# Kernel tuning notes

Measured on AMD Instinct MI355X. Metric: run time of the kernel, lower is better.

Reference implementation:

```python
import jax, jax.numpy as jnp
import numpy as np

N = 8192
F_IN = 256
F_OUT = 128
NEG_BIG = -9.0e15


def setup_inputs() -> dict:
    key = jax.random.key(0)
    k1, k2, k3, k4 = jax.random.split(key, 4)
    x = jax.random.normal(k1, (N, F_IN), dtype=jnp.float32)
    W = jax.random.normal(k2, (F_IN, F_OUT), dtype=jnp.float32) * 0.05
    a = jax.random.normal(k3, (2 * F_OUT, 1), dtype=jnp.float32) * 0.05
    adj = jax.random.randint(k4, (N, N), 0, 2, dtype=jnp.int32)
    return {"x": x, "W": W, "a": a, "adj": adj}


def reference(x, W, a, adj):
    # h = x @ W : [N, F_OUT]
    h = x @ W
    # Original builds [N, N, 2F] concat then matmuls with a. Since
    # a_input[i,j] = concat(h_i, h_j), the score is separable:
    # (a_input @ a)[i,j] = h_i . a[:F] + h_j . a[F:]
    a1 = a[:F_OUT, 0]   # [F_OUT]
    a2 = a[F_OUT:, 0]   # [F_OUT]
    s1 = h @ a1         # [N]
    s2 = h @ a2         # [N]
    e = jax.nn.leaky_relu(s1[:, None] + s2[None, :], negative_slope=0.2)
    e = jnp.where(adj > 0, e, jnp.float32(NEG_BIG))
    attention = jax.nn.softmax(e, axis=1)   # [N, N]
    h_prime = attention @ h                 # [N, F_OUT]
    return jax.nn.elu(h_prime)
```

## Files before the change

### kernel.cpp

```cpp
#include <hip/hip_runtime.h>
#include <math.h>

#define NN 8192

typedef __attribute__((ext_vector_type(8))) short short8;
typedef __attribute__((ext_vector_type(4))) short short4v;
typedef __attribute__((ext_vector_type(4))) float f32x4;
typedef __attribute__((ext_vector_type(4))) int int4v;

#define L2E 1.4426950408889634f

typedef __attribute__((address_space(3))) unsigned lds_u32;
typedef __attribute__((address_space(1))) unsigned g_u32;

__device__ __forceinline__ void gll16(const void* g, void* l) {
    __builtin_amdgcn_global_load_lds((const g_u32*)g, (lds_u32*)l, 16, 0, 0);
}

__device__ __forceinline__ short f2bf(float f) {
    union { float f; unsigned u; } v; v.f = f;
    unsigned r = v.u + 0x7fffu + ((v.u >> 16) & 1u);
    return (short)(r >> 16);
}

__device__ __forceinline__ f32x4 zero4() {
    f32x4 v; v[0] = 0.f; v[1] = 0.f; v[2] = 0.f; v[3] = 0.f; return v;
}

__global__ void k0_wt(const float* __restrict__ W, short* __restrict__ WT) {
    int idx = blockIdx.x * 256 + threadIdx.x;
    if (idx < 256 * 128) {
        int k = idx & 255;
        int f = idx >> 8;
        WT[f * 256 + k] = f2bf(W[k * 128 + f]);
    }
}

__global__ __launch_bounds__(128) void k1_h(
        const float* __restrict__ x, const short* __restrict__ WT,
        const float* __restrict__ a, short* __restrict__ hT,
        float* __restrict__ s1L2E, float* __restrict__ s2L2E) {
    const int w = threadIdx.x >> 6;
    const int l = threadIdx.x & 63;
    const int quad = l >> 4;
    const int fr = l & 15;
    const int i0 = blockIdx.x * 32 + w * 16;

    f32x4 acc[8];
#pragma unroll
    for (int t = 0; t < 8; ++t) acc[t] = zero4();

    const float* xrow = x + (size_t)(i0 + fr) * 256;
#pragma unroll
    for (int kk = 0; kk < 8; ++kk) {
        const int k0 = kk * 32 + quad * 8;
        f32x4 xa = *(const f32x4*)(xrow + k0);
        f32x4 xb = *(const f32x4*)(xrow + k0 + 4);
        short8 av;
#pragma unroll
        for (int e = 0; e < 4; ++e) { av[e] = f2bf(xa[e]); av[4 + e] = f2bf(xb[e]); }
#pragma unroll
        for (int t = 0; t < 8; ++t) {
            short8 bv = *(const short8*)(WT + (t * 16 + fr) * 256 + k0);
            acc[t] = __builtin_amdgcn_mfma_f32_16x16x32_bf16(av, bv, acc[t], 0, 0, 0);
        }
    }

    float s1p[4] = {0.f, 0.f, 0.f, 0.f};
    float s2p[4] = {0.f, 0.f, 0.f, 0.f};
#pragma unroll
    for (int t = 0; t < 8; ++t) {
        float a1v = a[t * 16 + fr];
        float a2v = a[128 + t * 16 + fr];
#pragma unroll
        for (int r = 0; r < 4; ++r) {
            s1p[r] += acc[t][r] * a1v;
            s2p[r] += acc[t][r] * a2v;
        }
    }
#pragma unroll
    for (int r = 0; r < 4; ++r) {
#pragma unroll
        for (int m = 1; m < 16; m <<= 1) {
            s1p[r] += __shfl_xor(s1p[r], m, 64);
            s2p[r] += __shfl_xor(s2p[r], m, 64);
        }
    }
    if (fr == 0) {
#pragma unroll
        for (int r = 0; r < 4; ++r) {
            const int i = i0 + quad * 4 + r;
            s1L2E[i] = s1p[r] * L2E;
            s2L2E[i] = s2p[r] * L2E;
        }
    }

#pragma unroll
    for (int t = 0; t < 8; ++t) {
        short4v hv;
#pragma unroll
        for (int r = 0; r < 4; ++r) hv[r] = f2bf(acc[t][r]);
        *(short4v*)(hT + (size_t)(t * 16 + fr) * NN + i0 + quad * 4) = hv;
    }
}

template<int JSPLIT, bool PARTIAL>
__global__ __launch_bounds__(256, 2) void k2_attn(
        const int* __restrict__ adj, const short* __restrict__ hT,
        const float* __restrict__ s1g, const float* __restrict__ s2g,
        float* __restrict__ pvp, float* __restrict__ zp,
        float* __restrict__ out) {
    constexpr int JW = NN / JSPLIT;
    constexpr int NSTEP = JW / 64;
    constexpr int BUFB = 33792;
    __shared__ __align__(16) char lds_c[2 * BUFB + 512];

    const int tid = threadIdx.x;
    const int w = tid >> 6;
    const int l = tid & 63;
    const int quad = l >> 4;
    const int fr = l & 15;
    const int rh = w >> 1;
    const int wj = w & 1;
    const int rb = blockIdx.x / JSPLIT;
    const int jb = blockIdx.x % JSPLIT;
    const int r64 = rb * 64;
    const int jbb = jb * JW;

    const float S0 = s1g[r64 + rh * 32 + fr];
    const float S1 = s1g[r64 + rh * 32 + 16 + fr];

    const char* hsrc[4];
    const char* asrc[4];
    {
        const char* hbase = (const char*)hT;
        const char* abase = (const char*)adj;
#pragma unroll
        for (int p = 0; p < 4; ++p) {
            const int off = w * 4096 + p * 1024 + l * 16;
            {
                const int row = off >> 7;
                const int colb = off & 127;
                hsrc[p] = hbase + (size_t)row * (NN * 2) + (size_t)jbb * 2
                        + (colb ^ ((row & 7) << 4));
            }
            {
                const int row = off >> 8;
                const int colb = off & 255;
                asrc[p] = abase + (size_t)(r64 + row) * (NN * 4) + (size_t)jbb * 4
                        + (colb ^ ((row & 7) << 4));
            }
        }
    }
    const char* csrc = (const char*)s2g + (size_t)jbb * 4 + l * 16;

    auto STAGE = [&](int jt, int buf) {
        jt = (jt < NSTEP) ? jt : NSTEP - 1;
        char* hd = lds_c + buf * BUFB + w * 4096;
        char* ad = lds_c + buf * BUFB + 16384 + w * 4096;
        char* cd = lds_c + buf * BUFB + 32768;
        const size_t hof = (size_t)jt * 128;
        const size_t aof = (size_t)jt * 256;
#pragma unroll
        for (int p = 0; p < 4; ++p) gll16(hsrc[p] + hof, hd + p * 1024);
#pragma unroll
        for (int p = 0; p < 4; ++p) gll16(asrc[p] + aof, ad + p * 1024);
        gll16(csrc + aof, cd);
    };

    f32x4 acc[2][8];
#pragma unroll
    for (int m = 0; m < 2; ++m)
#pragma unroll
        for (int t = 0; t < 8; ++t) acc[m][t] = zero4();
    float zacc0 = 0.f, zacc1 = 0.f;

    STAGE(0, 0); STAGE(1, 1);

    const int ar0 = rh * 32 + fr;
    const int ar1 = rh * 32 + 16 + fr;
    const unsigned aswz = (unsigned)((ar0 & 7) << 4);
    const unsigned a0 = (unsigned)(ar0 * 256 + wj * 128 + quad * 32);
    const unsigned a1 = (unsigned)(ar1 * 256 + wj * 128 + quad * 32);

    for (int t = 0; t < NSTEP; ++t) {
        const int cur = t & 1;
        asm volatile("s_waitcnt vmcnt(9)" ::: "memory");
        __builtin_amdgcn_s_barrier();
        __builtin_amdgcn_sched_barrier(0);

        const char* hb = lds_c + cur * BUFB;
        const char* ab = lds_c + cur * BUFB + 16384;
        const float* cb = (const float*)(lds_c + cur * BUFB + 32768);

        const int4v g00 = *(const int4v*)(ab + (a0 ^ aswz));
        const int4v g01 = *(const int4v*)(ab + ((a0 + 16) ^ aswz));
        const int4v g10 = *(const int4v*)(ab + (a1 ^ aswz));
        const int4v g11 = *(const int4v*)(ab + ((a1 + 16) ^ aswz));
        const f32x4 c0 = *(const f32x4*)((const char*)cb + wj * 128 + quad * 32);
        const f32x4 c1 = *(const f32x4*)((const char*)cb + wj * 128 + quad * 32 + 16);

        short8 pa0, pa1;
        {
            float zs0 = 0.f, zs1 = 0.f;
#pragma unroll
            for (int e = 0; e < 8; ++e) {
                const float cv = (e < 4) ? c0[e] : c1[e - 4];
                const int gv0 = (e < 4) ? g00[e] : g01[e - 4];
                const int gv1 = (e < 4) ? g10[e] : g11[e - 4];
                const float u0 = S0 + cv;
                const float u1 = S1 + cv;
                const float t0 = fmaxf(u0, 0.2f * u0);
                const float t1 = fmaxf(u1, 0.2f * u1);
                const float p0 = (gv0 > 0) ? exp2f(t0) : 0.f;
                const float p1 = (gv1 > 0) ? exp2f(t1) : 0.f;
                zs0 += p0; zs1 += p1;
                pa0[e] = f2bf(p0);
                pa1[e] = f2bf(p1);
            }
            zacc0 += zs0; zacc1 += zs1;
        }

#pragma unroll
        for (int t8 = 0; t8 < 8; ++t8) {
            const int hrow = t8 * 16 + fr;
            const short8 bv = *(const short8*)(
                hb + ((unsigned)(hrow * 128 + wj * 64 + quad * 16) ^ ((hrow & 7) << 4)));
            acc[0][t8] = __builtin_amdgcn_mfma_f32_16x16x32_bf16(pa0, bv, acc[0][t8], 0, 0, 0);
            acc[1][t8] = __builtin_amdgcn_mfma_f32_16x16x32_bf16(pa1, bv, acc[1][t8], 0, 0, 0);
        }

        __builtin_amdgcn_sched_barrier(0);
        __builtin_amdgcn_s_barrier();
        STAGE(t + 2, cur);
    }

    asm volatile("s_waitcnt vmcnt(0)" ::: "memory");
    __syncthreads();

    zacc0 += __shfl_xor(zacc0, 16, 64);
    zacc0 += __shfl_xor(zacc0, 32, 64);
    zacc1 += __shfl_xor(zacc1, 16, 64);
    zacc1 += __shfl_xor(zacc1, 32, 64);
    float* zb = (float*)(lds_c + 2 * BUFB);
    if (l < 16) {
        zb[w * 32 + l] = zacc0;
        zb[w * 32 + 16 + l] = zacc1;
    }

    float* red = (float*)lds_c;
    if (wj == 1) {
#pragma unroll
        for (int m = 0; m < 2; ++m)
#pragma unroll
            for (int t8 = 0; t8 < 8; ++t8)
                *(f32x4*)(red + rh * 4096 + (m * 8 + t8) * 256 + l * 4) = acc[m][t8];
    }
    __syncthreads();

    if (wj == 0) {
#pragma unroll
        for (int m = 0; m < 2; ++m)
#pragma unroll
            for (int t8 = 0; t8 < 8; ++t8)
                acc[m][t8] += *(const f32x4*)(red + rh * 4096 + (m * 8 + t8) * 256 + l * 4);
#pragma unroll
        for (int m = 0; m < 2; ++m) {
#pragma unroll
            for (int r = 0; r < 4; ++r) {
                const int rr = m * 16 + quad * 4 + r;
                const float z = zb[(rh * 2 + 0) * 32 + rr] + zb[(rh * 2 + 1) * 32 + rr];
                const int grow = r64 + rh * 32 + rr;
                if (PARTIAL) {
                    if (fr == 0) zp[(size_t)jb * NN + grow] = z;
                    float* orow = pvp + ((size_t)jb * NN + grow) * 128;
#pragma unroll
                    for (int t8 = 0; t8 < 8; ++t8) orow[t8 * 16 + fr] = acc[m][t8][r];
                } else {
                    const float inv = 1.0f / z;
                    float* orow = out + (size_t)grow * 128;
#pragma unroll
                    for (int t8 = 0; t8 < 8; ++t8) {
                        float v = acc[m][t8][r] * inv;
                        orow[t8 * 16 + fr] = (v > 0.f) ? v : expm1f(v);
                    }
                }
            }
        }
    }
}

__global__ __launch_bounds__(256) void k3_fin(
        const float* __restrict__ pvp, const float* __restrict__ zp,
        float* __restrict__ out, int jsplit) {
    const int idx = blockIdx.x * 256 + threadIdx.x;
    const int row = idx >> 5;
    const int c = (idx & 31) << 2;
    f32x4 s = zero4();
    float z = 0.f;
    for (int p = 0; p < jsplit; ++p) {
        s += *(const f32x4*)(pvp + ((size_t)p * NN + row) * 128 + c);
        z += zp[(size_t)p * NN + row];
    }
    const float inv = 1.0f / z;
    f32x4 o;
#pragma unroll
    for (int e = 0; e < 4; ++e) {
        float v = s[e] * inv;
        o[e] = (v > 0.f) ? v : expm1f(v);
    }
    *(f32x4*)(out + (size_t)row * 128 + c) = o;
}

extern "C" void kernel_launch(void* const* d_in, const int* in_sizes, int n_in,
                              void* d_out, int out_size, void* d_ws, size_t ws_size,
                              hipStream_t stream) {
    const float* x   = (const float*)d_in[0];
    const float* W   = (const float*)d_in[1];
    const float* a   = (const float*)d_in[2];
    const int*   adj = (const int*)d_in[3];
    float* out = (float*)d_out;

    char* ws = (char*)d_ws;
    const size_t MB = 1024 * 1024;
    short* hT    = (short*)ws;
    float* s1L2E = (float*)(ws + 2 * MB);
    float* s2L2E = (float*)(ws + 2 * MB + 32768);
    short* WT    = (short*)(ws + 2 * MB + 65536);
    const size_t base = 2 * MB + 131072;

    auto need = [&](size_t js) {
        return base + js * ((size_t)NN * 128 * 4) + js * ((size_t)NN * 4);
    };
    int jsplit;
    if (ws_size >= need(4)) jsplit = 4;
    else if (ws_size >= need(2)) jsplit = 2;
    else if (ws_size >= need(1)) jsplit = 1;
    else jsplit = 0;

    float* pvp = (float*)(ws + base);
    float* zp  = (float*)(ws + base + (size_t)(jsplit > 0 ? jsplit : 1) * NN * 128 * 4);

    k0_wt<<<128, 256, 0, stream>>>(W, WT);
    k1_h<<<256, 128, 0, stream>>>(x, WT, a, hT, s1L2E, s2L2E);

    if (jsplit == 4) {
        k2_attn<4, true><<<512, 256, 0, stream>>>(adj, hT, s1L2E, s2L2E, pvp, zp, nullptr);
        k3_fin<<<1024, 256, 0, stream>>>(pvp, zp, out, 4);
    } else if (jsplit == 2) {
        k2_attn<2, true><<<256, 256, 0, stream>>>(adj, hT, s1L2E, s2L2E, pvp, zp, nullptr);
        k3_fin<<<1024, 256, 0, stream>>>(pvp, zp, out, 2);
    } else if (jsplit == 1) {
        k2_attn<1, true><<<128, 256, 0, stream>>>(adj, hT, s1L2E, s2L2E, pvp, zp, nullptr);
        k3_fin<<<1024, 256, 0, stream>>>(pvp, zp, out, 1);
    } else {
        k2_attn<1, false><<<128, 256, 0, stream>>>(adj, hT, s1L2E, s2L2E, nullptr, nullptr, out);
    }
}
```

Baseline: 83.91 us.

## Pack adjacency into a bitmask in a separate pass before attention

Adds a pre-pass kernel that converts the int32 adjacency matrix into 32-bit bitmasks. The attention kernel then reads mask bits directly from global memory instead of staging int32 adjacency tiles through LDS. LDS use drops to a double-buffered h tile and occupancy is raised to three blocks per CU. The full adjacency read still happens in the pack kernel, and the change adds a launch plus more workspace, which could shift the split choice.

```diff
diff --git a/kernel.cpp b/kernel.cpp
--- a/kernel.cpp
+++ b/kernel.cpp
@@ -33,6 +33,26 @@
         int k = idx & 255;
         int f = idx >> 8;
         WT[f * 256 + k] = f2bf(W[k * 128 + f]);
+    }
+}
+
+__global__ __launch_bounds__(256) void k_pack(
+        const int* __restrict__ adj, unsigned* __restrict__ bm32) {
+    const size_t tid = (size_t)blockIdx.x * 256 + threadIdx.x;
+    const size_t nthr = (size_t)gridDim.x * 256;
+    const size_t NW = (size_t)NN * NN / 32;
+    for (size_t wdx = tid; wdx < NW; wdx += nthr) {
+        const int4v* p = (const int4v*)(adj + wdx * 32);
+        int4v v[8];
+#pragma unroll
+        for (int q = 0; q < 8; ++q) v[q] = p[q];
+        unsigned b = 0;
+#pragma unroll
+        for (int q = 0; q < 8; ++q)
+#pragma unroll
+            for (int e = 0; e < 4; ++e)
+                b |= (v[q][e] > 0 ? 1u : 0u) << (q * 4 + e);
+        bm32[wdx] = b;
     }
 }
 
@@ -105,15 +125,14 @@
 }
 
 template<int JSPLIT, bool PARTIAL>
-__global__ __launch_bounds__(256, 2) void k2_attn(
-        const int* __restrict__ adj, const short* __restrict__ hT,
+__global__ __launch_bounds__(256, 3) void k2_attn(
+        const unsigned* __restrict__ bm32, const short* __restrict__ hT,
         const float* __restrict__ s1g, const float* __restrict__ s2g,
         float* __restrict__ pvp, float* __restrict__ zp,
         float* __restrict__ out) {
     constexpr int JW = NN / JSPLIT;
     constexpr int NSTEP = JW / 64;
-    constexpr int BUFB = 33792;
-    __shared__ __align__(16) char lds_c[2 * BUFB + 512];
+    __shared__ __align__(16) char lds_c[32768 + 512];
 
     const int tid = threadIdx.x;
     const int w = tid >> 6;
@@ -127,46 +146,33 @@
     const int r64 = rb * 64;
     const int jbb = jb * JW;
 
-    const float S0 = s1g[r64 + rh * 32 + fr];
-    const float S1 = s1g[r64 + rh * 32 + 16 + fr];
+    const int ar0 = rh * 32 + fr;
+    const int ar1 = rh * 32 + 16 + fr;
+    const float S0 = s1g[r64 + ar0];
+    const float S1 = s1g[r64 + ar1];
 
     const char* hsrc[4];
-    const char* asrc[4];
     {
         const char* hbase = (const char*)hT;
-        const char* abase = (const char*)adj;
 #pragma unroll
         for (int p = 0; p < 4; ++p) {
             const int off = w * 4096 + p * 1024 + l * 16;
-            {
-                const int row = off >> 7;
-                const int colb = off & 127;
-                hsrc[p] = hbase + (size_t)row * (NN * 2) + (size_t)jbb * 2
-                        + (colb ^ ((row & 7) << 4));
-            }
-            {
-                const int row = off >> 8;
-                const int colb = off & 255;
-                asrc[p] = abase + (size_t)(r64 + row) * (NN * 4) + (size_t)jbb * 4
-                        + (colb ^ ((row & 7) << 4));
-            }
-        }
-    }
-    const char* csrc = (const char*)s2g + (size_t)jbb * 4 + l * 16;
-
-    auto STAGE = [&](int jt, int buf) {
-        jt = (jt < NSTEP) ? jt : NSTEP - 1;
-        char* hd = lds_c + buf * BUFB + w * 4096;
-        char* ad = lds_c + buf * BUFB + 16384 + w * 4096;
-        char* cd = lds_c + buf * BUFB + 32768;
+            const int row = off >> 7;
+            const int colb = off & 127;
+            hsrc[p] = hbase + (size_t)row * (NN * 2) + (size_t)jbb * 2
+                    + (colb ^ ((row & 7) << 4));
+        }
+    }
+    auto STAGE_HT = [&](int jt, int buf) {
+        char* hd = lds_c + buf * 16384 + w * 4096;
         const size_t hof = (size_t)jt * 128;
-        const size_t aof = (size_t)jt * 256;
 #pragma unroll
         for (int p = 0; p < 4; ++p) gll16(hsrc[p] + hof, hd + p * 1024);
-#pragma unroll
-        for (int p = 0; p < 4; ++p) gll16(asrc[p] + aof, ad + p * 1024);
-        gll16(csrc + aof, cd);
     };
+
+    const unsigned* m0p = bm32 + (size_t)(r64 + ar0) * (NN / 32) + jbb / 32;
+    const unsigned* m1p = bm32 + (size_t)(r64 + ar1) * (NN / 32) + jbb / 32;
+    const float* cbase = s2g + jbb + wj * 32 + quad * 8;
 
     f32x4 acc[2][8];
 #pragma unroll
@@ -175,45 +181,45 @@
         for (int t = 0; t < 8; ++t) acc[m][t] = zero4();
     float zacc0 = 0.f, zacc1 = 0.f;
 
-    STAGE(0, 0); STAGE(1, 1);
-
-    const int ar0 = rh * 32 + fr;
-    const int ar1 = rh * 32 + 16 + fr;
-    const unsigned aswz = (unsigned)((ar0 & 7) << 4);
-    const unsigned a0 = (unsigned)(ar0 * 256 + wj * 128 + quad * 32);
-    const unsigned a1 = (unsigned)(ar1 * 256 + wj * 128 + quad * 32);
+    STAGE_HT(0, 0);
+    int4v mk0c = *(const int4v*)(m0p);
+    int4v mk1c = *(const int4v*)(m1p);
+    int4v mk0n = mk0c, mk1n = mk1c;
+    f32x4 cc0 = *(const f32x4*)(cbase);
+    f32x4 cc1 = *(const f32x4*)(cbase + 4);
+    __syncthreads();
 
     for (int t = 0; t < NSTEP; ++t) {
-        const int cur = t & 1;
-        asm volatile("s_waitcnt vmcnt(9)" ::: "memory");
-        __builtin_amdgcn_s_barrier();
-        __builtin_amdgcn_sched_barrier(0);
-
-        const char* hb = lds_c + cur * BUFB;
-        const char* ab = lds_c + cur * BUFB + 16384;
-        const float* cb = (const float*)(lds_c + cur * BUFB + 32768);
-
-        const int4v g00 = *(const int4v*)(ab + (a0 ^ aswz));
-        const int4v g01 = *(const int4v*)(ab + ((a0 + 16) ^ aswz));
-        const int4v g10 = *(const int4v*)(ab + (a1 ^ aswz));
-        const int4v g11 = *(const int4v*)(ab + ((a1 + 16) ^ aswz));
-        const f32x4 c0 = *(const f32x4*)((const char*)cb + wj * 128 + quad * 32);
-        const f32x4 c1 = *(const f32x4*)((const char*)cb + wj * 128 + quad * 32 + 16);
+        if (t + 1 < NSTEP) STAGE_HT(t + 1, (t + 1) & 1);
+        if ((t & 1) == 0) {
+            const int tn = (t + 2 < NSTEP) ? t + 2 : NSTEP - 2;
+            mk0n = *(const int4v*)(m0p + tn * 2);
+            mk1n = *(const int4v*)(m1p + tn * 2);
+        }
+        f32x4 cn0, cn1;
+        {
+            const int tc = (t + 1 < NSTEP) ? t + 1 : NSTEP - 1;
+            cn0 = *(const f32x4*)(cbase + tc * 64);
+            cn1 = *(const f32x4*)(cbase + tc * 64 + 4);
+        }
+
+        const char* hb = lds_c + (t & 1) * 16384;
+
+        const unsigned bits0 = ((unsigned)mk0c[(t & 1) * 2 + wj] >> (quad * 8)) & 0xffu;
+        const unsigned bits1 = ((unsigned)mk1c[(t & 1) * 2 + wj] >> (quad * 8)) & 0xffu;
 
         short8 pa0, pa1;
         {
             float zs0 = 0.f, zs1 = 0.f;
 #pragma unroll
             for (int e = 0; e < 8; ++e) {
-                const float cv = (e < 4) ? c0[e] : c1[e - 4];
-                const int gv0 = (e < 4) ? g00[e] : g01[e - 4];
-                const int gv1 = (e < 4) ? g10[e] : g11[e - 4];
+                const float cv = (e < 4) ? cc0[e] : cc1[e - 4];
                 const float u0 = S0 + cv;
                 const float u1 = S1 + cv;
                 const float t0 = fmaxf(u0, 0.2f * u0);
                 const float t1 = fmaxf(u1, 0.2f * u1);
-                const float p0 = (gv0 > 0) ? exp2f(t0) : 0.f;
-                const float p1 = (gv1 > 0) ? exp2f(t1) : 0.f;
+                const float p0 = ((bits0 >> e) & 1u) ? exp2f(t0) : 0.f;
+                const float p1 = ((bits1 >> e) & 1u) ? exp2f(t1) : 0.f;
                 zs0 += p0; zs1 += p1;
                 pa0[e] = f2bf(p0);
                 pa1[e] = f2bf(p1);
@@ -230,19 +236,16 @@
             acc[1][t8] = __builtin_amdgcn_mfma_f32_16x16x32_bf16(pa1, bv, acc[1][t8], 0, 0, 0);
         }
 
-        __builtin_amdgcn_sched_barrier(0);
-        __builtin_amdgcn_s_barrier();
-        STAGE(t + 2, cur);
-    }
-
-    asm volatile("s_waitcnt vmcnt(0)" ::: "memory");
-    __syncthreads();
+        if (t & 1) { mk0c = mk0n; mk1c = mk1n; }
+        cc0 = cn0; cc1 = cn1;
+        __syncthreads();
+    }
 
     zacc0 += __shfl_xor(zacc0, 16, 64);
     zacc0 += __shfl_xor(zacc0, 32, 64);
     zacc1 += __shfl_xor(zacc1, 16, 64);
     zacc1 += __shfl_xor(zacc1, 32, 64);
-    float* zb = (float*)(lds_c + 2 * BUFB);
+    float* zb = (float*)(lds_c + 32768);
     if (l < 16) {
         zb[w * 32 + l] = zacc0;
         zb[w * 32 + 16 + l] = zacc1;
@@ -327,7 +330,8 @@
     float* s1L2E = (float*)(ws + 2 * MB);
     float* s2L2E = (float*)(ws + 2 * MB + 32768);
     short* WT    = (short*)(ws + 2 * MB + 65536);
-    const size_t base = 2 * MB + 131072;
+    unsigned* bm32 = (unsigned*)(ws + 2 * MB + 131072);
+    const size_t base = 2 * MB + 131072 + (size_t)NN * NN / 8;
 
     auto need = [&](size_t js) {
         return base + js * ((size_t)NN * 128 * 4) + js * ((size_t)NN * 4);
@@ -343,17 +347,18 @@
 
     k0_wt<<<128, 256, 0, stream>>>(W, WT);
     k1_h<<<256, 128, 0, stream>>>(x, WT, a, hT, s1L2E, s2L2E);
+    k_pack<<<2048, 256, 0, stream>>>(adj, bm32);
 
     if (jsplit == 4) {
-        k2_attn<4, true><<<512, 256, 0, stream>>>(adj, hT, s1L2E, s2L2E, pvp, zp, nullptr);
+        k2_attn<4, true><<<512, 256, 0, stream>>>(bm32, hT, s1L2E, s2L2E, pvp, zp, nullptr);
         k3_fin<<<1024, 256, 0, stream>>>(pvp, zp, out, 4);
     } else if (jsplit == 2) {
-        k2_attn<2, true><<<256, 256, 0, stream>>>(adj, hT, s1L2E, s2L2E, pvp, zp, nullptr);
+        k2_attn<2, true><<<256, 256, 0, stream>>>(bm32, hT, s1L2E, s2L2E, pvp, zp, nullptr);
         k3_fin<<<1024, 256, 0, stream>>>(pvp, zp, out, 2);
     } else if (jsplit == 1) {
-        k2_attn<1, true><<<128, 256, 0, stream>>>(adj, hT, s1L2E, s2L2E, pvp, zp, nullptr);
+        k2_attn<1, true><<<128, 256, 0, stream>>>(bm32, hT, s1L2E, s2L2E, pvp, zp, nullptr);
         k3_fin<<<1024, 256, 0, stream>>>(pvp, zp, out, 1);
     } else {
-        k2_attn<1, false><<<128, 256, 0, stream>>>(adj, hT, s1L2E, s2L2E, nullptr, nullptr, out);
-    }
-}
+        k2_attn<1, false><<<128, 256, 0, stream>>>(bm32, hT, s1L2E, s2L2E, nullptr, nullptr, out);
+    }
+}
```

Result: slower. 130.4 us (+55.4%).
